# Kernel tuning notes

Measured on AMD Instinct MI355X. Metric: run time of the kernel, lower is better.

Reference implementation:

```python
import jax, jax.numpy as jnp
import numpy as np
import math

NUM_EXPERTS = 8
CAP_FACTOR = 1.25
MIN_CAPACITY = 4

def _capacity(num_tokens, num_experts):
    cap = math.floor(CAP_FACTOR * num_tokens / num_experts)
    cap += cap % 2
    return max(cap, MIN_CAPACITY)

def setup_inputs() -> dict:
    key = jax.random.key(0)
    k1, k2, k3, k4 = jax.random.split(key, 4)
    tokens, d_model, d_ff, E = 8192, 1024, 4096, NUM_EXPERTS
    x = jax.random.normal(k1, (tokens, d_model), dtype=jnp.float32)
    gate_weight = jax.random.normal(k2, (E, d_model), dtype=jnp.float32) * math.sqrt(0.1 / d_model)
    expert_weight = jax.random.normal(k3, (E, d_model, d_ff), dtype=jnp.float32) * 0.02
    expert_bias = jax.random.normal(k4, (E, 1, d_ff), dtype=jnp.float32) * 0.02
    return {"x": x, "gate_weight": gate_weight, "expert_weight": expert_weight, "expert_bias": expert_bias}

def reference(x, gate_weight, expert_weight, expert_bias):
    tokens, d_model = x.shape
    E = gate_weight.shape[0]
    capacity = _capacity(tokens, E)
    # FP32 gate (Switch-style)
    gate_logits = jnp.dot(x.astype(jnp.float32), gate_weight.astype(jnp.float32).T)  # [s, E]
    logits = jax.nn.softmax(gate_logits, axis=-1)  # auto_cast_softmax in fp32
    # Top-1 routing, select_policy='first'
    top1_idx = jnp.argmax(gate_logits, axis=-1)  # argmax over raw gate output
    mask = jax.nn.one_hot(top1_idx, E, dtype=jnp.int32)  # [s, E]
    # aux load-balancing loss (training path)
    me = jnp.mean(logits, axis=0)
    ce = jnp.mean(mask.astype(jnp.float32), axis=0)
    l_aux = E * jnp.sum(me * ce)
    # cumsum-based capacity ranking
    ranks = jnp.cumsum(mask, axis=0) - 1  # [s, E]
    mask = mask * (ranks < capacity).astype(jnp.int32)
    ranks_tok = jnp.sum(mask * ranks, axis=-1)  # [s]
    rank_oh = jax.nn.one_hot(ranks_tok, capacity, dtype=logits.dtype)  # [s, c]
    weight = mask.astype(logits.dtype) * logits  # [s, E]
    combine_weights = weight[:, :, None] * rank_oh[:, None, :]  # [s, E, c]
    sec_mask = combine_weights != 0  # bool dispatch mask
    # scatter dispatch: [s,E,c] x [s,d] -> [E,c,d]
    dispatched = jnp.einsum("sec,sd->ecd", sec_mask.astype(x.dtype), x)
    # per-expert front linear: [E,c,d] x [E,d,f] -> [E,c,f]
    out = jnp.einsum("ecd,edf->ecf", dispatched, expert_weight) + expert_bias
    return out, combine_weights, l_aux
```

## Files before the change

### kernel.cpp

```cpp
#include <hip/hip_runtime.h>
#include <hip/hip_bf16.h>

#define TOKENS 8192
#define DM 1024
#define DFF 4096
#define NE 8
#define CAP 1280
#define ECAP (NE*CAP)
#define OUT_ELEMS ((size_t)NE*CAP*DFF)
#define CMB_ELEMS ((size_t)TOKENS*NE*CAP)
#define ZROW TOKENS
#define GBK 32

typedef __attribute__((ext_vector_type(8))) short short8;
typedef __attribute__((ext_vector_type(16))) float f32x16;
typedef __attribute__((ext_vector_type(4))) float f4;

__device__ inline ushort f2bf(float f) {
    __hip_bfloat16 h = __float2bfloat16(f);
    return *reinterpret_cast<ushort*>(&h);
}

__device__ __forceinline__ void gload16(const ushort* g, short* l) {
    __builtin_amdgcn_global_load_lds(
        (const __attribute__((address_space(1))) void*)g,
        (__attribute__((address_space(3))) void*)l, 16, 0, 0);
}

__global__ __launch_bounds__(256) void gate_kernel(const float* __restrict__ x,
        const float* __restrict__ gw, float* __restrict__ probs8, int* __restrict__ top1,
        ushort* __restrict__ xbf) {
    int wave = threadIdx.x >> 6;
    int lane = threadIdx.x & 63;
    int t = blockIdx.x * 4 + wave;
    const float* xrow = x + (size_t)t * DM;
    float4 xv[4];
    #pragma unroll
    for (int j = 0; j < 4; ++j) xv[j] = *(const float4*)(xrow + lane * 4 + j * 256);
    ushort* xbrow = xbf + (size_t)t * DM;
    #pragma unroll
    for (int j = 0; j < 4; ++j) {
        ushort4 o;
        o.x = f2bf(xv[j].x); o.y = f2bf(xv[j].y); o.z = f2bf(xv[j].z); o.w = f2bf(xv[j].w);
        *(ushort4*)(xbrow + lane * 4 + j * 256) = o;
    }
    float logit[8];
    #pragma unroll
    for (int e = 0; e < 8; ++e) {
        const float* g = gw + e * DM;
        float s = 0.f;
        #pragma unroll
        for (int j = 0; j < 4; ++j) {
            float4 gv = *(const float4*)(g + lane * 4 + j * 256);
            s += xv[j].x * gv.x + xv[j].y * gv.y + xv[j].z * gv.z + xv[j].w * gv.w;
        }
        #pragma unroll
        for (int off = 32; off >= 1; off >>= 1) s += __shfl_xor(s, off);
        logit[e] = s;
    }
    if (lane == 0) {
        int bi = 0; float bv = logit[0];
        #pragma unroll
        for (int e = 1; e < 8; ++e) if (logit[e] > bv) { bv = logit[e]; bi = e; }
        float se = 0.f, p[8];
        #pragma unroll
        for (int e = 0; e < 8; ++e) { p[e] = expf(logit[e] - bv); se += p[e]; }
        float inv = 1.f / se;
        #pragma unroll
        for (int e = 0; e < 8; ++e) probs8[t * 8 + e] = p[e] * inv;
        top1[t] = bi;
    }
    if (blockIdx.x == 0) {
        ushort4 z; z.x = z.y = z.z = z.w = 0;
        *(ushort4*)(xbf + (size_t)ZROW * DM + threadIdx.x * 4) = z;
    }
}

__global__ __launch_bounds__(512) void cvtw_rank_kernel(
        const float* __restrict__ w, ushort* __restrict__ wt,
        const int* __restrict__ top1, const float* __restrict__ probs8,
        int* __restrict__ slot_token, int* __restrict__ pos,
        int* __restrict__ cnts, float* __restrict__ laux_out) {
    __shared__ __align__(16) char smem[TOKENS * 4 + 64 * 4 + 8 * 4];
    const int tid = threadIdx.x;
    if (blockIdx.x == 0) {
        int* t1s = (int*)smem;
        float* red = (float*)(smem + TOKENS * 4);
        int* cnt_sh = (int*)(smem + TOKENS * 4 + 64 * 4);
        int w8 = tid >> 6;
        int lane = tid & 63;
        for (int i = tid; i < TOKENS; i += 512) t1s[i] = top1[i];
        for (int i = tid; i < ECAP; i += 512) slot_token[i] = ZROW;
        for (int i = tid; i < TOKENS; i += 512) pos[i] = -1;

        float ps[8];
        #pragma unroll
        for (int e = 0; e < 8; ++e) ps[e] = 0.f;
        for (int t = tid; t < TOKENS; t += 512) {
            float4 a = *(const float4*)(probs8 + t * 8);
            float4 b = *(const float4*)(probs8 + t * 8 + 4);
            ps[0] += a.x; ps[1] += a.y; ps[2] += a.z; ps[3] += a.w;
            ps[4] += b.x; ps[5] += b.y; ps[6] += b.z; ps[7] += b.w;
        }
        #pragma unroll
        for (int e = 0; e < 8; ++e) {
            #pragma unroll
            for (int off = 32; off >= 1; off >>= 1) ps[e] += __shfl_xor(ps[e], off);
        }
        if (lane == 0) {
            #pragma unroll
            for (int e = 0; e < 8; ++e) red[w8 * 8 + e] = ps[e];
        }
        __syncthreads();

        int base = 0;
        for (int t0 = 0; t0 < TOKENS; t0 += 256) {
            #pragma unroll
            for (int q = 0; q < 4; ++q) {
                int t = t0 + q * 64 + lane;
                bool mine = (t1s[t] == w8);
                unsigned long long m = __ballot(mine);
                if (mine) {
                    int r = base + __popcll(m & ((1ull << lane) - 1ull));
                    if (r < CAP) { slot_token[w8 * CAP + r] = t; pos[t] = w8 * CAP + r; }
                }
                base += __popcll(m);
            }
        }
        if (lane == 0) { cnt_sh[w8] = base; cnts[w8] = (base < CAP) ? base : CAP; }
        __syncthreads();
        if (tid == 0) {
            float la = 0.f;
            #pragma unroll
            for (int e = 0; e < 8; ++e) {
                float me = 0.f;
                #pragma unroll
                for (int wv = 0; wv < 8; ++wv) me += red[wv * 8 + e];
                la += (me / (float)TOKENS) * ((float)cnt_sh[e] / (float)TOKENS);
            }
            laux_out[0] = la * (float)NE;
        }
        return;
    }
    float (*tile)[65] = (float(*)[65])smem;
    int b = blockIdx.x - 1;
    int e = b >> 11;
    int rem = b & 2047;
    int n0 = (rem & 63) * 64;
    int k0 = (rem >> 6) * 32;
    const float* we = w + (size_t)e * DM * DFF;
    int c = tid & 63, r0 = tid >> 6;
    #pragma unroll
    for (int i = 0; i < 4; ++i) {
        int r = r0 + i * 8;
        tile[r][c] = we[(size_t)(k0 + r) * DFF + n0 + c];
    }
    __syncthreads();
    ushort* wte = wt + (size_t)e * DFF * DM;
    int kc = tid & 31, nr0 = tid >> 5;
    #pragma unroll
    for (int i = 0; i < 4; ++i) {
        int nr = nr0 + i * 16;
        wte[(size_t)(n0 + nr) * DM + k0 + kc] = f2bf(tile[kc][nr]);
    }
}

__global__ __launch_bounds__(512, 4) void gemm_kernel(
    const ushort* __restrict__ xbf,
    const ushort* __restrict__ wt,
    const float*  __restrict__ bias,
    const int*    __restrict__ slot_token,
    const int*    __restrict__ cnts,
    float* __restrict__ out,
    const int*    __restrict__ pos,
    const float*  __restrict__ probs8,
    float* __restrict__ cmb,
    int do_combine)
{
    const int bid = blockIdx.x;
    const int e   = bid & 7;
    const int rem = bid >> 3;
    const int nt  = rem & 31;
    const int mt  = rem >> 5;
    __shared__ __align__(16) short lds[3][12288];
    const int tid  = threadIdx.x;
    const int lane = tid & 63;
    const int wave = tid >> 6;
    const int wr = wave >> 1;
    const int wc = wave & 1;
    const int ln31 = lane & 31, lh = lane >> 5;
    const int tbeg = bid * 8;
    const bool has_cmb = do_combine && (bid < 1024);

    float* orow = out + ((size_t)(e * CAP + mt * 256)) * DFF + (size_t)nt * 128;

    f4* cmb_p = (f4*)cmb + (size_t)tbeg * (ECAP / 4);
    int kpart = 0, ntok = 0;
    int cur_p = -1, nxt_p = -1;
    float cur_val = 0.f, nxt_val = 0.f;
    if (has_cmb) {
        cur_p = pos[tbeg];
        { int ee = (cur_p < 0) ? 0 : (cur_p / CAP); cur_val = probs8[tbeg * 8 + ee]; }
        nxt_p = pos[tbeg + 1];
        { int ee = (nxt_p < 0) ? 0 : (nxt_p / CAP); nxt_val = probs8[(tbeg + 1) * 8 + ee]; }
    }
    #define CSTORE() do { \
        int c_ = tid + kpart * 512; \
        int b4_ = c_ * 4; \
        f4 v_; \
        v_.x = (b4_ + 0 == cur_p) ? cur_val : 0.f; \
        v_.y = (b4_ + 1 == cur_p) ? cur_val : 0.f; \
        v_.z = (b4_ + 2 == cur_p) ? cur_val : 0.f; \
        v_.w = (b4_ + 3 == cur_p) ? cur_val : 0.f; \
        __builtin_nontemporal_store(v_, cmb_p + c_); \
        if (++kpart == 5) { \
            kpart = 0; cmb_p += ECAP / 4; ++ntok; \
            cur_p = nxt_p; cur_val = nxt_val; \
            if (ntok + 1 < 8) { \
                nxt_p = pos[tbeg + ntok + 1]; \
                int ee_ = (nxt_p < 0) ? 0 : (nxt_p / CAP); \
                nxt_val = probs8[(tbeg + ntok + 1) * 8 + ee_]; \
            } \
        } \
    } while (0)

    if (mt * 256 >= cnts[e]) {
        int c4 = tid & 31;
        int r0b = tid >> 5;
        f4 bv4 = *(const f4*)(bias + e * DFF + nt * 128 + c4 * 4);
        for (int r = r0b; r < 256; r += 16)
            __builtin_nontemporal_store(bv4, (f4*)(orow + (size_t)r * DFF + c4 * 4));
        if (has_cmb) { while (ntok < 8) CSTORE(); }
        return;
    }

    const int r0a = tid >> 2;
    const int kg = (tid & 3) ^ ((tid >> 3) & 3);
    const int tokA0 = slot_token[e * CAP + mt * 256 + r0a];
    const int tokA1 = slot_token[e * CAP + mt * 256 + 128 + r0a];
    const ushort* aptr0 = xbf + (size_t)tokA0 * DM + kg * 8;
    const ushort* aptr1 = xbf + (size_t)tokA1 * DM + kg * 8;
    const ushort* bptr  = wt + ((size_t)e * DFF + (size_t)nt * 128 + r0a) * DM + kg * 8;

    #define STAGE(T, BUF) do { \
        short* base_ = &lds[BUF][0]; \
        size_t ko_ = (size_t)(T) * GBK; \
        gload16(aptr0 + ko_, base_ + tid * 8); \
        gload16(aptr1 + ko_, base_ + 4096 + tid * 8); \
        gload16(bptr  + ko_, base_ + 8192 + tid * 8); \
    } while (0)

    int aoff[4], boff[4];
    #pragma unroll
    for (int s = 0; s < 2; ++s) {
        #pragma unroll
        for (int mi = 0; mi < 2; ++mi) {
            int r = wr * 64 + mi * 32 + ln31;
            int c = lh + 2 * s;
            aoff[s * 2 + mi] = (r * 4 + (c ^ ((r >> 1) & 3))) * 8;
        }
        #pragma unroll
        for (int ni = 0; ni < 2; ++ni) {
            int rn = wc * 64 + ni * 32 + ln31;
            int c = lh + 2 * s;
            boff[s * 2 + ni] = 8192 + (rn * 4 + (c ^ ((rn >> 1) & 3))) * 8;
        }
    }

    f32x16 acc[2][2];
    #pragma unroll
    for (int mi = 0; mi < 2; ++mi)
        #pragma unroll
        for (int ni = 0; ni < 2; ++ni)
            acc[mi][ni] = (f32x16)(0.f);

    STAGE(0, 0); STAGE(1, 1);
    int cur = 0;
    int nxt2 = 2;
    #define KLOOP(W0, W1, WS, W30, W31, DOCMB) \
    for (int t = 0; t < 32; ++t) { \
        if (t < 30) STAGE(t + 2, nxt2); \
        if (t == 0)       asm volatile("s_waitcnt vmcnt(" #W0 ")" ::: "memory"); \
        else if (t == 1)  asm volatile("s_waitcnt vmcnt(" #W1 ")" ::: "memory"); \
        else if (t < 30)  asm volatile("s_waitcnt vmcnt(" #WS ")" ::: "memory"); \
        else if (t == 30) asm volatile("s_waitcnt vmcnt(" #W30 ")" ::: "memory"); \
        else              asm volatile("s_waitcnt vmcnt(" #W31 ")" ::: "memory"); \
        __builtin_amdgcn_s_barrier();            \
        __builtin_amdgcn_sched_barrier(0); \
        { \
            const short* L = &lds[cur][0]; \
            __builtin_amdgcn_s_setprio(1); \
            _Pragma("unroll") \
            for (int s = 0; s < 2; ++s) { \
                short8 af[2], bfr[2]; \
                _Pragma("unroll") \
                for (int ni = 0; ni < 2; ++ni) bfr[ni] = *(const short8*)(L + boff[s * 2 + ni]); \
                _Pragma("unroll") \
                for (int mi = 0; mi < 2; ++mi) af[mi] = *(const short8*)(L + aoff[s * 2 + mi]); \
                _Pragma("unroll") \
                for (int mi = 0; mi < 2; ++mi) \
                    _Pragma("unroll") \
                    for (int ni = 0; ni < 2; ++ni) \
                        acc[mi][ni] = __builtin_amdgcn_mfma_f32_32x32x16_bf16(af[mi], bfr[ni], acc[mi][ni], 0, 0, 0); \
            } \
            __builtin_amdgcn_s_setprio(0); \
        } \
        if (DOCMB) CSTORE();                     \
        __builtin_amdgcn_sched_barrier(0); \
        asm volatile("" ::: "memory"); \
        __builtin_amdgcn_s_barrier();            \
        asm volatile("" ::: "memory"); \
        cur = (cur == 2) ? 0 : cur + 1; \
        nxt2 = (nxt2 == 2) ? 0 : nxt2 + 1; \
    }

    if (has_cmb) {
        KLOOP(6, 7, 8, 5, 2, 1);
    } else {
        KLOOP(6, 6, 6, 3, 0, 0);
    }
    #undef KLOOP
    #undef STAGE

    #pragma unroll
    for (int ni = 0; ni < 2; ++ni) {
        int c = wc * 64 + ni * 32 + ln31;
        float bv = bias[e * DFF + nt * 128 + c];
        #pragma unroll
        for (int mi = 0; mi < 2; ++mi) {
            #pragma unroll
            for (int reg = 0; reg < 16; ++reg) {
                int r = wr * 64 + mi * 32 + (reg & 3) + 8 * (reg >> 2) + 4 * lh;
                __builtin_nontemporal_store(acc[mi][ni][reg] + bv,
                    orow + (size_t)r * DFF + c);
            }
        }
    }
    if (has_cmb) { while (ntok < 8) CSTORE(); }
    #undef CSTORE
}

__global__ __launch_bounds__(256) void combine_kernel(const int* __restrict__ pos,
        const float* __restrict__ probs8, float* __restrict__ cmb) {
    int tok = blockIdx.x;
    int p = pos[tok];
    int e = p / CAP;
    float val = probs8[tok * 8 + (e < 0 ? 0 : e)];
    f4* row = (f4*)(cmb + (size_t)tok * ECAP);
    #pragma unroll
    for (int k = 0; k < 10; ++k) {
        int c = threadIdx.x + k * 256;
        int b4 = c * 4;
        f4 v;
        v.x = (b4 + 0 == p) ? val : 0.f;
        v.y = (b4 + 1 == p) ? val : 0.f;
        v.z = (b4 + 2 == p) ? val : 0.f;
        v.w = (b4 + 3 == p) ? val : 0.f;
        __builtin_nontemporal_store(v, row + c);
    }
}

extern "C" void kernel_launch(void* const* d_in, const int* in_sizes, int n_in,
                              void* d_out, int out_size, void* d_ws, size_t ws_size,
                              hipStream_t stream) {
    const float* x  = (const float*)d_in[0];
    const float* gw = (const float*)d_in[1];
    const float* ew = (const float*)d_in[2];
    const float* eb = (const float*)d_in[3];

    float* out = (float*)d_out;
    float* cmb = out + OUT_ELEMS;
    float* laux_out = cmb + CMB_ELEMS;

    float* probs8 = (float*)d_ws;
    int* top1 = (int*)(probs8 + TOKENS * 8);
    int* slot_token = top1 + TOKENS;
    int* pos = slot_token + ECAP;
    int* cnts = pos + TOKENS;

    const size_t SMALL = 1 << 20;
    const size_t WT_ELEMS_ = (size_t)NE * DFF * DM;
    const size_t XBF_ELEMS_ = (size_t)(TOKENS + 1) * DM;
    bool big_ws = ws_size >= SMALL + (WT_ELEMS_ + XBF_ELEMS_) * sizeof(ushort);
    ushort* wtbf = big_ws ? (ushort*)((char*)d_ws + SMALL) : (ushort*)cmb;
    ushort* xbf  = wtbf + WT_ELEMS_;

    gate_kernel<<<TOKENS / 4, 256, 0, stream>>>(x, gw, probs8, top1, xbf);
    cvtw_rank_kernel<<<16385, 512, 0, stream>>>(ew, wtbf, top1, probs8,
                                                slot_token, pos, cnts, laux_out);
    if (big_ws) {
        gemm_kernel<<<1280, 512, 0, stream>>>(xbf, wtbf, eb, slot_token, cnts, out,
                                              pos, probs8, cmb, 1);
    } else {
        gemm_kernel<<<1280, 512, 0, stream>>>(xbf, wtbf, eb, slot_token, cnts, out,
                                              pos, probs8, cmb, 0);
        combine_kernel<<<TOKENS, 256, 0, stream>>>(pos, probs8, cmb);
    }
}
```

Measured before the change: 187.5 us.

## Fuse gate and weight-convert/rank kernels using an atomic completion counter

```diff
diff --git a/kernel.cpp b/kernel.cpp
--- a/kernel.cpp
+++ b/kernel.cpp
@@ -11,6 +11,8 @@
 #define CMB_ELEMS ((size_t)TOKENS*NE*CAP)
 #define ZROW TOKENS
 #define GBK 32
+#define NGATE 1024
+#define NCVT 16384
 
 typedef __attribute__((ext_vector_type(8))) short short8;
 typedef __attribute__((ext_vector_type(16))) float f32x16;
@@ -27,63 +29,77 @@
         (__attribute__((address_space(3))) void*)l, 16, 0, 0);
 }
 
-__global__ __launch_bounds__(256) void gate_kernel(const float* __restrict__ x,
-        const float* __restrict__ gw, float* __restrict__ probs8, int* __restrict__ top1,
-        ushort* __restrict__ xbf) {
-    int wave = threadIdx.x >> 6;
-    int lane = threadIdx.x & 63;
-    int t = blockIdx.x * 4 + wave;
-    const float* xrow = x + (size_t)t * DM;
-    float4 xv[4];
-    #pragma unroll
-    for (int j = 0; j < 4; ++j) xv[j] = *(const float4*)(xrow + lane * 4 + j * 256);
-    ushort* xbrow = xbf + (size_t)t * DM;
-    #pragma unroll
-    for (int j = 0; j < 4; ++j) {
-        ushort4 o;
-        o.x = f2bf(xv[j].x); o.y = f2bf(xv[j].y); o.z = f2bf(xv[j].z); o.w = f2bf(xv[j].w);
-        *(ushort4*)(xbrow + lane * 4 + j * 256) = o;
-    }
-    float logit[8];
-    #pragma unroll
-    for (int e = 0; e < 8; ++e) {
-        const float* g = gw + e * DM;
-        float s = 0.f;
-        #pragma unroll
-        for (int j = 0; j < 4; ++j) {
-            float4 gv = *(const float4*)(g + lane * 4 + j * 256);
-            s += xv[j].x * gv.x + xv[j].y * gv.y + xv[j].z * gv.z + xv[j].w * gv.w;
-        }
-        #pragma unroll
-        for (int off = 32; off >= 1; off >>= 1) s += __shfl_xor(s, off);
-        logit[e] = s;
-    }
-    if (lane == 0) {
-        int bi = 0; float bv = logit[0];
-        #pragma unroll
-        for (int e = 1; e < 8; ++e) if (logit[e] > bv) { bv = logit[e]; bi = e; }
-        float se = 0.f, p[8];
-        #pragma unroll
-        for (int e = 0; e < 8; ++e) { p[e] = expf(logit[e] - bv); se += p[e]; }
-        float inv = 1.f / se;
-        #pragma unroll
-        for (int e = 0; e < 8; ++e) probs8[t * 8 + e] = p[e] * inv;
-        top1[t] = bi;
-    }
-    if (blockIdx.x == 0) {
-        ushort4 z; z.x = z.y = z.z = z.w = 0;
-        *(ushort4*)(xbf + (size_t)ZROW * DM + threadIdx.x * 4) = z;
-    }
-}
-
-__global__ __launch_bounds__(512) void cvtw_rank_kernel(
+__global__ __launch_bounds__(512) void fused_k1(
+        const float* __restrict__ x, const float* __restrict__ gw,
         const float* __restrict__ w, ushort* __restrict__ wt,
-        const int* __restrict__ top1, const float* __restrict__ probs8,
+        float* __restrict__ probs8, int* __restrict__ top1,
+        ushort* __restrict__ xbf,
         int* __restrict__ slot_token, int* __restrict__ pos,
-        int* __restrict__ cnts, float* __restrict__ laux_out) {
+        int* __restrict__ cnts, float* __restrict__ laux_out,
+        int* __restrict__ counter) {
     __shared__ __align__(16) char smem[TOKENS * 4 + 64 * 4 + 8 * 4];
     const int tid = threadIdx.x;
-    if (blockIdx.x == 0) {
+    const int bid = blockIdx.x;
+
+    if (bid >= 1 && bid <= NGATE) {
+        int wave = tid >> 6;
+        int lane = tid & 63;
+        int t = (bid - 1) * 8 + wave;
+        const float* xrow = x + (size_t)t * DM;
+        float4 xv[4];
+        #pragma unroll
+        for (int j = 0; j < 4; ++j) xv[j] = *(const float4*)(xrow + lane * 4 + j * 256);
+        ushort* xbrow = xbf + (size_t)t * DM;
+        #pragma unroll
+        for (int j = 0; j < 4; ++j) {
+            ushort4 o;
+            o.x = f2bf(xv[j].x); o.y = f2bf(xv[j].y); o.z = f2bf(xv[j].z); o.w = f2bf(xv[j].w);
+            *(ushort4*)(xbrow + lane * 4 + j * 256) = o;
+        }
+        float logit[8];
+        #pragma unroll
+        for (int e = 0; e < 8; ++e) {
+            const float* g = gw + e * DM;
+            float s = 0.f;
+            #pragma unroll
+            for (int j = 0; j < 4; ++j) {
+                float4 gv = *(const float4*)(g + lane * 4 + j * 256);
+                s += xv[j].x * gv.x + xv[j].y * gv.y + xv[j].z * gv.z + xv[j].w * gv.w;
+            }
+            #pragma unroll
+            for (int off = 32; off >= 1; off >>= 1) s += __shfl_xor(s, off);
+            logit[e] = s;
+        }
+        if (lane == 0) {
+            int bi = 0; float bv = logit[0];
+            #pragma unroll
+            for (int e = 1; e < 8; ++e) if (logit[e] > bv) { bv = logit[e]; bi = e; }
+            float se = 0.f, p[8];
+            #pragma unroll
+            for (int e = 0; e < 8; ++e) { p[e] = expf(logit[e] - bv); se += p[e]; }
+            float inv = 1.f / se;
+            #pragma unroll
+            for (int e = 0; e < 8; ++e) probs8[t * 8 + e] = p[e] * inv;
+            top1[t] = bi;
+        }
+        if (bid == 1 && tid < 256) {
+            ushort4 z; z.x = z.y = z.z = z.w = 0;
+            *(ushort4*)(xbf + (size_t)ZROW * DM + tid * 4) = z;
+        }
+        __threadfence();
+        __syncthreads();
+        if (tid == 0)
+            __hip_atomic_fetch_add(counter, 1, __ATOMIC_RELEASE, __HIP_MEMORY_SCOPE_AGENT);
+        return;
+    }
+
+    if (bid == 0) {
+        if (tid == 0) {
+            while (__hip_atomic_load(counter, __ATOMIC_ACQUIRE, __HIP_MEMORY_SCOPE_AGENT) < NGATE)
+                __builtin_amdgcn_s_sleep(8);
+        }
+        __syncthreads();
+
         int* t1s = (int*)smem;
         float* red = (float*)(smem + TOKENS * 4);
         int* cnt_sh = (int*)(smem + TOKENS * 4 + 64 * 4);
@@ -142,8 +158,9 @@
         }
         return;
     }
+
     float (*tile)[65] = (float(*)[65])smem;
-    int b = blockIdx.x - 1;
+    int b = bid - (NGATE + 1);
     int e = b >> 11;
     int rem = b & 2047;
     int n0 = (rem & 63) * 64;
@@ -377,6 +394,7 @@
     int* slot_token = top1 + TOKENS;
     int* pos = slot_token + ECAP;
     int* cnts = pos + TOKENS;
+    int* counter = cnts + 8;
 
     const size_t SMALL = 1 << 20;
     const size_t WT_ELEMS_ = (size_t)NE * DFF * DM;
@@ -385,9 +403,9 @@
     ushort* wtbf = big_ws ? (ushort*)((char*)d_ws + SMALL) : (ushort*)cmb;
     ushort* xbf  = wtbf + WT_ELEMS_;
 
-    gate_kernel<<<TOKENS / 4, 256, 0, stream>>>(x, gw, probs8, top1, xbf);
-    cvtw_rank_kernel<<<16385, 512, 0, stream>>>(ew, wtbf, top1, probs8,
-                                                slot_token, pos, cnts, laux_out);
+    hipMemsetAsync(counter, 0, sizeof(int), stream);
+    fused_k1<<<1 + NGATE + NCVT, 512, 0, stream>>>(x, gw, ew, wtbf, probs8, top1,
+            xbf, slot_token, pos, cnts, laux_out, counter);
     if (big_ws) {
         gemm_kernel<<<1280, 512, 0, stream>>>(xbf, wtbf, eb, slot_token, cnts, out,
                                               pos, probs8, cmb, 1);
```

Result: slower. 394.2 us (+110.2%).

## Fuse fp32 weight conversion into GEMM B-operand loading, drop transpose pre-pass

Applied to the files above, without the earlier changes.

```diff
diff --git a/kernel.cpp b/kernel.cpp
--- a/kernel.cpp
+++ b/kernel.cpp
@@ -21,6 +21,8 @@
     return *reinterpret_cast<ushort*>(&h);
 }
 
+union U8C { short8 s; ushort u[8]; };
+
 __device__ __forceinline__ void gload16(const ushort* g, short* l) {
     __builtin_amdgcn_global_load_lds(
         (const __attribute__((address_space(1))) void*)g,
@@ -76,98 +78,71 @@
     }
 }
 
-__global__ __launch_bounds__(512) void cvtw_rank_kernel(
-        const float* __restrict__ w, ushort* __restrict__ wt,
-        const int* __restrict__ top1, const float* __restrict__ probs8,
-        int* __restrict__ slot_token, int* __restrict__ pos,
-        int* __restrict__ cnts, float* __restrict__ laux_out) {
-    __shared__ __align__(16) char smem[TOKENS * 4 + 64 * 4 + 8 * 4];
+__global__ __launch_bounds__(512) void rank_kernel(const int* __restrict__ top1,
+        const float* __restrict__ probs8, int* __restrict__ slot_token,
+        int* __restrict__ pos, int* __restrict__ cnts, float* __restrict__ laux_out) {
+    int w8 = threadIdx.x >> 6;
+    int lane = threadIdx.x & 63;
     const int tid = threadIdx.x;
-    if (blockIdx.x == 0) {
-        int* t1s = (int*)smem;
-        float* red = (float*)(smem + TOKENS * 4);
-        int* cnt_sh = (int*)(smem + TOKENS * 4 + 64 * 4);
-        int w8 = tid >> 6;
-        int lane = tid & 63;
-        for (int i = tid; i < TOKENS; i += 512) t1s[i] = top1[i];
-        for (int i = tid; i < ECAP; i += 512) slot_token[i] = ZROW;
-        for (int i = tid; i < TOKENS; i += 512) pos[i] = -1;
-
-        float ps[8];
-        #pragma unroll
-        for (int e = 0; e < 8; ++e) ps[e] = 0.f;
-        for (int t = tid; t < TOKENS; t += 512) {
-            float4 a = *(const float4*)(probs8 + t * 8);
-            float4 b = *(const float4*)(probs8 + t * 8 + 4);
-            ps[0] += a.x; ps[1] += a.y; ps[2] += a.z; ps[3] += a.w;
-            ps[4] += b.x; ps[5] += b.y; ps[6] += b.z; ps[7] += b.w;
-        }
+    __shared__ int t1s[TOKENS];
+    __shared__ float red[64];
+    __shared__ int cnt_sh[8];
+    for (int i = tid; i < TOKENS; i += 512) t1s[i] = top1[i];
+    for (int i = tid; i < ECAP; i += 512) slot_token[i] = ZROW;
+    for (int i = tid; i < TOKENS; i += 512) pos[i] = -1;
+
+    float ps[8];
+    #pragma unroll
+    for (int e = 0; e < 8; ++e) ps[e] = 0.f;
+    for (int t = tid; t < TOKENS; t += 512) {
+        float4 a = *(const float4*)(probs8 + t * 8);
+        float4 b = *(const float4*)(probs8 + t * 8 + 4);
+        ps[0] += a.x; ps[1] += a.y; ps[2] += a.z; ps[3] += a.w;
+        ps[4] += b.x; ps[5] += b.y; ps[6] += b.z; ps[7] += b.w;
+    }
+    #pragma unroll
+    for (int e = 0; e < 8; ++e) {
+        #pragma unroll
+        for (int off = 32; off >= 1; off >>= 1) ps[e] += __shfl_xor(ps[e], off);
+    }
+    if (lane == 0) {
+        #pragma unroll
+        for (int e = 0; e < 8; ++e) red[w8 * 8 + e] = ps[e];
+    }
+    __syncthreads();
+
+    int base = 0;
+    for (int t0 = 0; t0 < TOKENS; t0 += 256) {
+        #pragma unroll
+        for (int q = 0; q < 4; ++q) {
+            int t = t0 + q * 64 + lane;
+            bool mine = (t1s[t] == w8);
+            unsigned long long m = __ballot(mine);
+            if (mine) {
+                int r = base + __popcll(m & ((1ull << lane) - 1ull));
+                if (r < CAP) { slot_token[w8 * CAP + r] = t; pos[t] = w8 * CAP + r; }
+            }
+            base += __popcll(m);
+        }
+    }
+    if (lane == 0) { cnt_sh[w8] = base; cnts[w8] = (base < CAP) ? base : CAP; }
+    __syncthreads();
+    if (tid == 0) {
+        float la = 0.f;
         #pragma unroll
         for (int e = 0; e < 8; ++e) {
-            #pragma unroll
-            for (int off = 32; off >= 1; off >>= 1) ps[e] += __shfl_xor(ps[e], off);
-        }
-        if (lane == 0) {
-            #pragma unroll
-            for (int e = 0; e < 8; ++e) red[w8 * 8 + e] = ps[e];
-        }
-        __syncthreads();
-
-        int base = 0;
-        for (int t0 = 0; t0 < TOKENS; t0 += 256) {
-            #pragma unroll
-            for (int q = 0; q < 4; ++q) {
-                int t = t0 + q * 64 + lane;
-                bool mine = (t1s[t] == w8);
-                unsigned long long m = __ballot(mine);
-                if (mine) {
-                    int r = base + __popcll(m & ((1ull << lane) - 1ull));
-                    if (r < CAP) { slot_token[w8 * CAP + r] = t; pos[t] = w8 * CAP + r; }
-                }
-                base += __popcll(m);
-            }
-        }
-        if (lane == 0) { cnt_sh[w8] = base; cnts[w8] = (base < CAP) ? base : CAP; }
-        __syncthreads();
-        if (tid == 0) {
-            float la = 0.f;
-            #pragma unroll
-            for (int e = 0; e < 8; ++e) {
-                float me = 0.f;
-                #pragma unroll
-                for (int wv = 0; wv < 8; ++wv) me += red[wv * 8 + e];
-                la += (me / (float)TOKENS) * ((float)cnt_sh[e] / (float)TOKENS);
-            }
-            laux_out[0] = la * (float)NE;
-        }
-        return;
-    }
-    float (*tile)[65] = (float(*)[65])smem;
-    int b = blockIdx.x - 1;
-    int e = b >> 11;
-    int rem = b & 2047;
-    int n0 = (rem & 63) * 64;
-    int k0 = (rem >> 6) * 32;
-    const float* we = w + (size_t)e * DM * DFF;
-    int c = tid & 63, r0 = tid >> 6;
-    #pragma unroll
-    for (int i = 0; i < 4; ++i) {
-        int r = r0 + i * 8;
-        tile[r][c] = we[(size_t)(k0 + r) * DFF + n0 + c];
-    }
-    __syncthreads();
-    ushort* wte = wt + (size_t)e * DFF * DM;
-    int kc = tid & 31, nr0 = tid >> 5;
-    #pragma unroll
-    for (int i = 0; i < 4; ++i) {
-        int nr = nr0 + i * 16;
-        wte[(size_t)(n0 + nr) * DM + k0 + kc] = f2bf(tile[kc][nr]);
+            float me = 0.f;
+            #pragma unroll
+            for (int wv = 0; wv < 8; ++wv) me += red[wv * 8 + e];
+            la += (me / (float)TOKENS) * ((float)cnt_sh[e] / (float)TOKENS);
+        }
+        laux_out[0] = la * (float)NE;
     }
 }
 
 __global__ __launch_bounds__(512, 4) void gemm_kernel(
     const ushort* __restrict__ xbf,
-    const ushort* __restrict__ wt,
+    const float*  __restrict__ w,
     const float*  __restrict__ bias,
     const int*    __restrict__ slot_token,
     const int*    __restrict__ cnts,
@@ -240,14 +215,27 @@
     const int tokA1 = slot_token[e * CAP + mt * 256 + 128 + r0a];
     const ushort* aptr0 = xbf + (size_t)tokA0 * DM + kg * 8;
     const ushort* aptr1 = xbf + (size_t)tokA1 * DM + kg * 8;
-    const ushort* bptr  = wt + ((size_t)e * DFF + (size_t)nt * 128 + r0a) * DM + kg * 8;
-
-    #define STAGE(T, BUF) do { \
-        short* base_ = &lds[BUF][0]; \
+    const float* bsrc = w + (size_t)e * DM * DFF + (size_t)(kg * 8) * DFF
+                          + (size_t)nt * 128 + r0a;
+
+    #define STAGE_A(T) do { \
+        short* base_ = &lds[(T) % 3][0]; \
         size_t ko_ = (size_t)(T) * GBK; \
         gload16(aptr0 + ko_, base_ + tid * 8); \
         gload16(aptr1 + ko_, base_ + 4096 + tid * 8); \
-        gload16(bptr  + ko_, base_ + 8192 + tid * 8); \
+    } while (0)
+
+    float br[8];
+    #define BLOAD(T) do { \
+        const float* bp_ = bsrc + (size_t)(T) * GBK * DFF; \
+        _Pragma("unroll") \
+        for (int j = 0; j < 8; ++j) br[j] = bp_[(size_t)j * DFF]; \
+    } while (0)
+    #define BWRITE(T) do { \
+        U8C u_; \
+        _Pragma("unroll") \
+        for (int j = 0; j < 8; ++j) u_.u[j] = f2bf(br[j]); \
+        *(short8*)(&lds[(T) % 3][8192 + tid * 8]) = u_.s; \
     } while (0)
 
     int aoff[4], boff[4];
@@ -274,53 +262,43 @@
         for (int ni = 0; ni < 2; ++ni)
             acc[mi][ni] = (f32x16)(0.f);
 
-    STAGE(0, 0); STAGE(1, 1);
-    int cur = 0;
-    int nxt2 = 2;
-    #define KLOOP(W0, W1, WS, W30, W31, DOCMB) \
-    for (int t = 0; t < 32; ++t) { \
-        if (t < 30) STAGE(t + 2, nxt2); \
-        if (t == 0)       asm volatile("s_waitcnt vmcnt(" #W0 ")" ::: "memory"); \
-        else if (t == 1)  asm volatile("s_waitcnt vmcnt(" #W1 ")" ::: "memory"); \
-        else if (t < 30)  asm volatile("s_waitcnt vmcnt(" #WS ")" ::: "memory"); \
-        else if (t == 30) asm volatile("s_waitcnt vmcnt(" #W30 ")" ::: "memory"); \
-        else              asm volatile("s_waitcnt vmcnt(" #W31 ")" ::: "memory"); \
-        __builtin_amdgcn_s_barrier();            \
-        __builtin_amdgcn_sched_barrier(0); \
-        { \
-            const short* L = &lds[cur][0]; \
-            __builtin_amdgcn_s_setprio(1); \
-            _Pragma("unroll") \
-            for (int s = 0; s < 2; ++s) { \
-                short8 af[2], bfr[2]; \
-                _Pragma("unroll") \
-                for (int ni = 0; ni < 2; ++ni) bfr[ni] = *(const short8*)(L + boff[s * 2 + ni]); \
-                _Pragma("unroll") \
-                for (int mi = 0; mi < 2; ++mi) af[mi] = *(const short8*)(L + aoff[s * 2 + mi]); \
-                _Pragma("unroll") \
-                for (int mi = 0; mi < 2; ++mi) \
-                    _Pragma("unroll") \
-                    for (int ni = 0; ni < 2; ++ni) \
-                        acc[mi][ni] = __builtin_amdgcn_mfma_f32_32x32x16_bf16(af[mi], bfr[ni], acc[mi][ni], 0, 0, 0); \
-            } \
-            __builtin_amdgcn_s_setprio(0); \
-        } \
-        if (DOCMB) CSTORE();                     \
-        __builtin_amdgcn_sched_barrier(0); \
-        asm volatile("" ::: "memory"); \
-        __builtin_amdgcn_s_barrier();            \
-        asm volatile("" ::: "memory"); \
-        cur = (cur == 2) ? 0 : cur + 1; \
-        nxt2 = (nxt2 == 2) ? 0 : nxt2 + 1; \
-    }
-
-    if (has_cmb) {
-        KLOOP(6, 7, 8, 5, 2, 1);
-    } else {
-        KLOOP(6, 6, 6, 3, 0, 0);
-    }
-    #undef KLOOP
-    #undef STAGE
+    STAGE_A(0); BLOAD(0); STAGE_A(1);
+    BWRITE(0);
+    BLOAD(1);
+
+    for (int t = 0; t < 32; ++t) {
+        if (t < 30) STAGE_A(t + 2);
+        if (t < 31) BWRITE(t + 1);
+        if (t < 30) BLOAD(t + 2);
+        asm volatile("s_waitcnt lgkmcnt(0)" ::: "memory");
+        __builtin_amdgcn_s_barrier();
+        __builtin_amdgcn_sched_barrier(0);
+
+        const short* L = &lds[t % 3][0];
+        __builtin_amdgcn_s_setprio(1);
+        #pragma unroll
+        for (int s = 0; s < 2; ++s) {
+            short8 af[2], bfr[2];
+            #pragma unroll
+            for (int ni = 0; ni < 2; ++ni) bfr[ni] = *(const short8*)(L + boff[s * 2 + ni]);
+            #pragma unroll
+            for (int mi = 0; mi < 2; ++mi) af[mi] = *(const short8*)(L + aoff[s * 2 + mi]);
+            #pragma unroll
+            for (int mi = 0; mi < 2; ++mi)
+                #pragma unroll
+                for (int ni = 0; ni < 2; ++ni)
+                    acc[mi][ni] = __builtin_amdgcn_mfma_f32_32x32x16_bf16(af[mi], bfr[ni], acc[mi][ni], 0, 0, 0);
+        }
+        __builtin_amdgcn_s_setprio(0);
+        if (has_cmb) CSTORE();
+        __builtin_amdgcn_sched_barrier(0);
+        asm volatile("" ::: "memory");
+        __builtin_amdgcn_s_barrier();
+        asm volatile("" ::: "memory");
+    }
+    #undef STAGE_A
+    #undef BLOAD
+    #undef BWRITE
 
     #pragma unroll
     for (int ni = 0; ni < 2; ++ni) {
@@ -379,20 +357,17 @@
     int* cnts = pos + TOKENS;
 
     const size_t SMALL = 1 << 20;
-    const size_t WT_ELEMS_ = (size_t)NE * DFF * DM;
     const size_t XBF_ELEMS_ = (size_t)(TOKENS + 1) * DM;
-    bool big_ws = ws_size >= SMALL + (WT_ELEMS_ + XBF_ELEMS_) * sizeof(ushort);
-    ushort* wtbf = big_ws ? (ushort*)((char*)d_ws + SMALL) : (ushort*)cmb;
-    ushort* xbf  = wtbf + WT_ELEMS_;
+    bool big_ws = ws_size >= SMALL + XBF_ELEMS_ * sizeof(ushort);
+    ushort* xbf = big_ws ? (ushort*)((char*)d_ws + SMALL) : (ushort*)cmb;
 
     gate_kernel<<<TOKENS / 4, 256, 0, stream>>>(x, gw, probs8, top1, xbf);
-    cvtw_rank_kernel<<<16385, 512, 0, stream>>>(ew, wtbf, top1, probs8,
-                                                slot_token, pos, cnts, laux_out);
+    rank_kernel<<<1, 512, 0, stream>>>(top1, probs8, slot_token, pos, cnts, laux_out);
     if (big_ws) {
-        gemm_kernel<<<1280, 512, 0, stream>>>(xbf, wtbf, eb, slot_token, cnts, out,
+        gemm_kernel<<<1280, 512, 0, stream>>>(xbf, ew, eb, slot_token, cnts, out,
                                               pos, probs8, cmb, 1);
     } else {
-        gemm_kernel<<<1280, 512, 0, stream>>>(xbf, wtbf, eb, slot_token, cnts, out,
+        gemm_kernel<<<1280, 512, 0, stream>>>(xbf, ew, eb, slot_token, cnts, out,
                                               pos, probs8, cmb, 0);
         combine_kernel<<<TOKENS, 256, 0, stream>>>(pos, probs8, cmb);
     }
```

Measured after the change: 215.9 us. 15.1% more time.
